# Optimization experiments

Hardware: AMD Instinct MI355X
Metric: run time of the kernel (lower is better)

The kernel has to match this reference:

```python
import jax, jax.numpy as jnp
import numpy as np

N_ENT, N_USR, N_ITEM, N_REL, N_CLS, N_FAC, D = 100000, 4096, 8192, 32, 3, 8, 128
N_EDGES, NNZ = 800000, 204800


def setup_inputs() -> dict:
    key = jax.random.key(0)
    ks = jax.random.split(key, 15)
    return {
        "entity_emb": jax.random.normal(ks[0], (N_ENT, D), jnp.float32),
        "item_emb": jax.random.normal(ks[1], (N_ITEM, D), jnp.float32),
        "user_emb": jax.random.normal(ks[2], (N_USR, D), jnp.float32),
        "latent_emb": jax.random.normal(ks[3], (N_FAC, D), jnp.float32),
        "relation_emb": jax.random.normal(ks[4], (N_REL, D), jnp.float32),
        "edge_index": jax.random.randint(ks[5], (2, N_EDGES), 0, N_ENT, jnp.int32),
        "edge_type": jax.random.randint(ks[6], (N_EDGES,), 0, N_REL, jnp.int32),
        "edge_imp": jax.random.uniform(ks[7], (N_EDGES,), jnp.float32),
        "inter_rows": jax.random.randint(ks[8], (NNZ,), 0, N_USR, jnp.int32),
        "inter_cols": jax.random.randint(ks[9], (NNZ,), 0, N_ENT, jnp.int32),
        "inter_vals": jax.random.uniform(ks[10], (NNZ,), jnp.float32),
        "disen_weight_att": jax.random.normal(ks[11], (N_FAC, N_REL), jnp.float32),
        "ent_rel_w": jax.random.normal(ks[12], (N_REL, D), jnp.float32),
        "usr_cls_w": jax.random.normal(ks[13], (N_CLS, D), jnp.float32),
        "inter_cls_mat": jax.random.normal(ks[14], (N_CLS, N_USR, N_ITEM), jnp.float32),
    }


def reference(entity_emb, item_emb, user_emb, latent_emb, relation_emb,
              edge_index, edge_type, edge_imp, inter_rows, inter_cols,
              inter_vals, disen_weight_att, ent_rel_w, usr_cls_w, inter_cls_mat):
    n_entities = entity_emb.shape[0]
    n_users = user_emb.shape[0]
    head, tail = edge_index[0], edge_index[1]

    # --- entity aggregation, e_mode='att_imp' ---
    # per-entity attention over relations: [n_ent, n_rel]
    ent_rel_att = jax.nn.softmax(entity_emb @ relation_emb.T, axis=1)
    mess_att = ent_rel_att[head, edge_type][:, None]              # [E,1]
    message_score = relation_emb[edge_type] * mess_att * edge_imp[:, None]  # [E,D]
    message = entity_emb[tail] * message_score                    # [E,D]
    entity_agg = jax.ops.segment_sum(message, head, num_segments=n_entities)

    # --- user aggregation, u_mode='inter_cls' ---
    # sparse interact_mat @ entity_emb via COO gather + segment_sum
    user_agg = jax.ops.segment_sum(entity_emb[inter_cols] * inter_vals[:, None],
                                   inter_rows, num_segments=n_users)
    user_cls_att = jax.nn.softmax(user_emb @ usr_cls_w.T, axis=1)  # [U,C]
    item_emb_2 = item_emb * relation_emb.sum(axis=0, keepdims=True)  # [I,D]
    # stack_c(inter_cls_mat[c] @ item_emb_2).transpose(0,1) -> [U,C,D]
    disen_weight = jnp.einsum('cui,id->ucd', inter_cls_mat, item_emb_2)
    user_agg = user_agg + (disen_weight * user_cls_att[:, :, None]).sum(axis=1)

    return entity_agg, user_agg
```

## Files before the change

kernel.cpp:

```cpp
#include <hip/hip_runtime.h>

#define N_ENT   100000
#define N_USR   4096
#define N_ITEM  8192
#define N_REL   32
#define N_CLS   3
#define DD      128
#define N_EDGES 800000
#define NNZ     204800

#define CAP_E   64
#define CAP_U   128

typedef __attribute__((ext_vector_type(8))) short short8;
typedef __attribute__((ext_vector_type(4))) float f32x4;

static __device__ __forceinline__ unsigned short f2bf(float x) {
    unsigned int u = __builtin_bit_cast(unsigned int, x);
    u = (u + 0x7fffu + ((u >> 16) & 1u)) >> 16;
    return (unsigned short)u;
}
static __device__ __forceinline__ float bflo(unsigned int v) {
    return __uint_as_float(v << 16);
}
static __device__ __forceinline__ float bfhi(unsigned int v) {
    return __uint_as_float(v & 0xffff0000u);
}

#define ZB  ((N_ENT + N_USR + 255) / 256)
#define EAB ((N_ENT + 255) / 256)

__global__ __launch_bounds__(256) void k_prep(const float* __restrict__ ent,
                                              const float* __restrict__ rel,
                                              float* __restrict__ att,
                                              unsigned short* __restrict__ entbf,
                                              unsigned short* __restrict__ relbf,
                                              int* __restrict__ cnt,
                                              const float* __restrict__ item,
                                              unsigned short* __restrict__ Bt,
                                              const float* __restrict__ usr,
                                              const float* __restrict__ w,
                                              float* __restrict__ uatt) {
    __shared__ float smem[N_REL * DD];
    int bx = blockIdx.x;

    if (bx < ZB) {
        int i = bx * 256 + threadIdx.x;
        if (i < N_ENT + N_USR) cnt[i] = 0;
        return;
    }
    bx -= ZB;

    if (bx < EAB) {
        for (int i = threadIdx.x; i < N_REL * DD; i += 256) smem[i] = rel[i];
        __syncthreads();
        if (bx == 0) {
            for (int i = threadIdx.x; i < N_REL * DD; i += 256)
                relbf[i] = f2bf(smem[i]);
        }
        int e = bx * 256 + threadIdx.x;
        if (e >= N_ENT) return;
        const float4* row = (const float4*)(ent + (size_t)e * DD);
        unsigned short* brow = entbf + (size_t)e * DD;
        float acc[N_REL];
#pragma unroll
        for (int r = 0; r < N_REL; ++r) acc[r] = 0.f;
        for (int dq = 0; dq < DD / 4; ++dq) {
            float4 v = row[dq];
            ushort4 bv;
            bv.x = f2bf(v.x); bv.y = f2bf(v.y); bv.z = f2bf(v.z); bv.w = f2bf(v.w);
            *(ushort4*)(brow + dq * 4) = bv;
#pragma unroll
            for (int r = 0; r < N_REL; ++r) {
                float4 ww = *(const float4*)&smem[r * DD + dq * 4];
                acc[r] += v.x * ww.x + v.y * ww.y + v.z * ww.z + v.w * ww.w;
            }
        }
        float m = acc[0];
#pragma unroll
        for (int r = 1; r < N_REL; ++r) m = fmaxf(m, acc[r]);
        float s = 0.f;
#pragma unroll
        for (int r = 0; r < N_REL; ++r) { acc[r] = __expf(acc[r] - m); s += acc[r]; }
        float inv = 1.f / s;
        float* o = att + (size_t)e * N_REL;
#pragma unroll
        for (int r = 0; r < N_REL; ++r) o[r] = acc[r] * inv;
        return;
    }
    bx -= EAB;

    if (bx < 1024) {
        float (*tile)[33] = (float(*)[33])smem;
        float* ssum = smem + 32 * 33;
        const int b2 = bx & 255, by = bx >> 8;
        const int tx = threadIdx.x & 31, ty = threadIdx.x >> 5;
        const int i0 = b2 * 32, d0 = by * 32;
        if (threadIdx.x < 32) {
            float s = 0.f;
            for (int r = 0; r < N_REL; ++r) s += rel[r * DD + d0 + threadIdx.x];
            ssum[threadIdx.x] = s;
        }
#pragma unroll
        for (int rr = 0; rr < 4; ++rr)
            tile[ty + 8 * rr][tx] = item[(size_t)(i0 + ty + 8 * rr) * DD + d0 + tx];
        __syncthreads();
#pragma unroll
        for (int rr = 0; rr < 4; ++rr) {
            int d = d0 + ty + 8 * rr;
            Bt[(size_t)d * N_ITEM + i0 + tx] = f2bf(tile[tx][ty + 8 * rr] * ssum[ty + 8 * rr]);
        }
        return;
    }
    bx -= 1024;

    {
        for (int i = threadIdx.x; i < N_CLS * DD; i += 256) smem[i] = w[i];
        __syncthreads();
        int u = bx * 256 + threadIdx.x;
        const float4* row = (const float4*)(usr + (size_t)u * DD);
        float acc[3] = {0.f, 0.f, 0.f};
        for (int dq = 0; dq < DD / 4; ++dq) {
            float4 v = row[dq];
#pragma unroll
            for (int c = 0; c < 3; ++c) {
                float4 ww = *(const float4*)&smem[c * DD + dq * 4];
                acc[c] += v.x * ww.x + v.y * ww.y + v.z * ww.z + v.w * ww.w;
            }
        }
        float m = fmaxf(acc[0], fmaxf(acc[1], acc[2]));
        float s = 0.f;
#pragma unroll
        for (int c = 0; c < 3; ++c) { acc[c] = __expf(acc[c] - m); s += acc[c]; }
        float inv = 1.f / s;
#pragma unroll
        for (int c = 0; c < 3; ++c) uatt[u * 3 + c] = acc[c] * inv;
    }
}

__global__ __launch_bounds__(256) void k_scatter2(const int* __restrict__ eidx,
                                                  const int* __restrict__ etyp,
                                                  const float* __restrict__ eimp,
                                                  const int* __restrict__ irow,
                                                  const int* __restrict__ icol,
                                                  const float* __restrict__ ival,
                                                  int* __restrict__ cnt,
                                                  int2* __restrict__ pack_e,
                                                  int2* __restrict__ pack_u) {
    int i = blockIdx.x * 256 + threadIdx.x;
    if (i < N_EDGES) {
        int h = eidx[i], tl = eidx[N_EDGES + i], r = etyp[i];
        int p = atomicAdd(&cnt[h], 1);
        if (p < CAP_E) {
            int2 pk;
            pk.x = tl | (r << 24);
            pk.y = __float_as_int(eimp[i]);
            pack_e[(size_t)h * CAP_E + p] = pk;
        }
    }
    if (i < NNZ) {
        int u = irow[i];
        int p = atomicAdd(&cnt[N_ENT + u], 1);
        if (p < CAP_U) {
            int2 pk;
            pk.x = icol[i];
            pk.y = __float_as_int(ival[i]);
            pack_u[(size_t)u * CAP_U + p] = pk;
        }
    }
}

__global__ __launch_bounds__(256) void k_edge_agg4(const unsigned short* __restrict__ entbf,
                                                   const unsigned short* __restrict__ relbf,
                                                   const float* __restrict__ att,
                                                   const int2* __restrict__ pack,
                                                   const int* __restrict__ cnt,
                                                   float* __restrict__ out) {
    const int lane = threadIdx.x & 63;
    const int wid = blockIdx.x * 4 + (threadIdx.x >> 6);
#pragma unroll 1
    for (int hh = 0; hh < 4; ++hh) {
        const int h = wid * 4 + hh;
        const int n = min(cnt[h], CAP_E);
        const float attv = att[(size_t)h * N_REL + (lane & 31)];
        const int2* seg = pack + (size_t)h * CAP_E;
        float ax = 0.f, ay = 0.f;
        for (int j = 0; j < n; j += 8) {
            int2 pk[8];
#pragma unroll
            for (int k = 0; k < 8; ++k) pk[k] = seg[min(j + k, n - 1)];
            unsigned int bv[8], rv[8];
            float sc[8];
#pragma unroll
            for (int k = 0; k < 8; ++k) {
                int r = ((unsigned)pk[k].x) >> 24;
                float s = __shfl(attv, r, 64) * __int_as_float(pk[k].y);
                sc[k] = (j + k < n) ? s : 0.f;
                bv[k] = ((const unsigned int*)(entbf + (size_t)(pk[k].x & 0xFFFFFF) * DD))[lane];
                rv[k] = ((const unsigned int*)(relbf + (size_t)r * DD))[lane];
            }
#pragma unroll
            for (int k = 0; k < 8; ++k) {
                ax = fmaf(bflo(rv[k]) * bflo(bv[k]), sc[k], ax);
                ay = fmaf(bfhi(rv[k]) * bfhi(bv[k]), sc[k], ay);
            }
        }
        float2 o; o.x = ax; o.y = ay;
        ((float2*)(out + (size_t)h * DD))[lane] = o;
    }
}

#define BM 64
#define BK 32
#define SPLITK 16
#define KCH (N_ITEM / SPLITK)
#define PLANE ((long long)N_USR * N_ITEM)

__global__ __launch_bounds__(256) void k_disen_gemm(const float* __restrict__ icm,
                                                    const unsigned short* __restrict__ Bt,
                                                    const float* __restrict__ uatt,
                                                    float* __restrict__ part) {
    __shared__ unsigned short sA[BM][40];
    __shared__ unsigned short sB[DD][40];

    const int t  = threadIdx.x;
    const int m0 = blockIdx.x * BM;
    const long long k0b = (long long)blockIdx.y * KCH;

    const int ua = t >> 3;
    const int qa = t & 7;
    const float a00 = uatt[(m0 + ua) * 3 + 0];
    const float a01 = uatt[(m0 + ua) * 3 + 1];
    const float a02 = uatt[(m0 + ua) * 3 + 2];
    const float a10 = uatt[(m0 + ua + 32) * 3 + 0];
    const float a11 = uatt[(m0 + ua + 32) * 3 + 1];
    const float a12 = uatt[(m0 + ua + 32) * 3 + 2];

    const int db = t >> 2;
    const int qb = t & 3;

    const int lane = t & 63;
    const int wv = t >> 6;
    const int wm = wv >> 1, wn = wv & 1;
    const int la = lane & 15, lb = lane >> 4;

    f32x4 acc[2][4];
#pragma unroll
    for (int mi = 0; mi < 2; ++mi)
#pragma unroll
        for (int ni = 0; ni < 4; ++ni) {
            f32x4 z = {0.f, 0.f, 0.f, 0.f};
            acc[mi][ni] = z;
        }

    float4 rA0[3], rA1[3];
    short8 rB0, rB1;
    {
        const long long base0 = (long long)(m0 + ua) * N_ITEM + k0b + qa * 4;
        rA0[0] = *(const float4*)(icm + base0);
        rA0[1] = *(const float4*)(icm + base0 + PLANE);
        rA0[2] = *(const float4*)(icm + base0 + 2 * PLANE);
        const long long base1 = base0 + 32ll * N_ITEM;
        rA1[0] = *(const float4*)(icm + base1);
        rA1[1] = *(const float4*)(icm + base1 + PLANE);
        rA1[2] = *(const float4*)(icm + base1 + 2 * PLANE);
        const unsigned short* g0 = Bt + (long long)db * N_ITEM + k0b + qb * 8;
        rB0 = *(const short8*)g0;
        rB1 = *(const short8*)(g0 + 64ll * N_ITEM);
    }

    for (int kk = 0; kk < KCH; kk += BK) {
        __syncthreads();
        {
            ushort4 p;
            p.x = f2bf(a00 * rA0[0].x + a01 * rA0[1].x + a02 * rA0[2].x);
            p.y = f2bf(a00 * rA0[0].y + a01 * rA0[1].y + a02 * rA0[2].y);
            p.z = f2bf(a00 * rA0[0].z + a01 * rA0[1].z + a02 * rA0[2].z);
            p.w = f2bf(a00 * rA0[0].w + a01 * rA0[1].w + a02 * rA0[2].w);
            *(ushort4*)(&sA[ua][0] + qa * 4) = p;
            p.x = f2bf(a10 * rA1[0].x + a11 * rA1[1].x + a12 * rA1[2].x);
            p.y = f2bf(a10 * rA1[0].y + a11 * rA1[1].y + a12 * rA1[2].y);
            p.z = f2bf(a10 * rA1[0].z + a11 * rA1[1].z + a12 * rA1[2].z);
            p.w = f2bf(a10 * rA1[0].w + a11 * rA1[1].w + a12 * rA1[2].w);
            *(ushort4*)(&sA[ua + 32][0] + qa * 4) = p;
            *(short8*)(&sB[db][0] + qb * 8) = rB0;
            *(short8*)(&sB[db + 64][0] + qb * 8) = rB1;
        }
        __syncthreads();

        if (kk + BK < KCH) {
            const long long k0 = k0b + kk + BK;
            const long long base0 = (long long)(m0 + ua) * N_ITEM + k0 + qa * 4;
            rA0[0] = *(const float4*)(icm + base0);
            rA0[1] = *(const float4*)(icm + base0 + PLANE);
            rA0[2] = *(const float4*)(icm + base0 + 2 * PLANE);
            const long long base1 = base0 + 32ll * N_ITEM;
            rA1[0] = *(const float4*)(icm + base1);
            rA1[1] = *(const float4*)(icm + base1 + PLANE);
            rA1[2] = *(const float4*)(icm + base1 + 2 * PLANE);
            const unsigned short* g0 = Bt + (long long)db * N_ITEM + k0 + qb * 8;
            rB0 = *(const short8*)g0;
            rB1 = *(const short8*)(g0 + 64ll * N_ITEM);
        }

        short8 af[2], bfr[4];
#pragma unroll
        for (int mi = 0; mi < 2; ++mi)
            af[mi] = *(const short8*)(&sA[wm * 32 + mi * 16 + la][0] + lb * 8);
#pragma unroll
        for (int ni = 0; ni < 4; ++ni)
            bfr[ni] = *(const short8*)(&sB[wn * 64 + ni * 16 + la][0] + lb * 8);
#pragma unroll
        for (int mi = 0; mi < 2; ++mi)
#pragma unroll
            for (int ni = 0; ni < 4; ++ni)
                acc[mi][ni] = __builtin_amdgcn_mfma_f32_16x16x32_bf16(
                    af[mi], bfr[ni], acc[mi][ni], 0, 0, 0);
    }

    float* pbase = part + (size_t)blockIdx.y * ((size_t)N_USR * DD);
#pragma unroll
    for (int mi = 0; mi < 2; ++mi)
#pragma unroll
        for (int ni = 0; ni < 4; ++ni)
#pragma unroll
            for (int r = 0; r < 4; ++r) {
                int row = m0 + wm * 32 + mi * 16 + lb * 4 + r;
                int col = wn * 64 + ni * 16 + la;
                pbase[(size_t)row * DD + col] = acc[mi][ni][r];
            }
}

__global__ __launch_bounds__(256) void k_user_final(const unsigned short* __restrict__ entbf,
                                                    const int2* __restrict__ pack,
                                                    const int* __restrict__ cnt,
                                                    const float* __restrict__ part,
                                                    float* __restrict__ uout) {
    const int lane = threadIdx.x & 63;
    const int u = blockIdx.x * 4 + (threadIdx.x >> 6);
    const int n = min(cnt[N_ENT + u], CAP_U);
    const int2* seg = pack + (size_t)u * CAP_U;
    float ax = 0.f, ay = 0.f;
    for (int j = 0; j < n; j += 8) {
        int2 pk[8];
#pragma unroll
        for (int k = 0; k < 8; ++k) pk[k] = seg[min(j + k, n - 1)];
        unsigned int bv[8];
        float sc[8];
#pragma unroll
        for (int k = 0; k < 8; ++k) {
            sc[k] = (j + k < n) ? __int_as_float(pk[k].y) : 0.f;
            bv[k] = ((const unsigned int*)(entbf + (size_t)pk[k].x * DD))[lane];
        }
#pragma unroll
        for (int k = 0; k < 8; ++k) {
            ax = fmaf(bflo(bv[k]), sc[k], ax);
            ay = fmaf(bfhi(bv[k]), sc[k], ay);
        }
    }
#pragma unroll
    for (int k = 0; k < SPLITK; ++k) {
        float2 p = ((const float2*)(part + (size_t)k * N_USR * DD + (size_t)u * DD))[lane];
        ax += p.x;
        ay += p.y;
    }
    float2 o; o.x = ax; o.y = ay;
    ((float2*)(uout + (size_t)u * DD))[lane] = o;
}

static constexpr size_t algn(size_t x) { return (x + 255) & ~(size_t)255; }

extern "C" void kernel_launch(void* const* d_in, const int* in_sizes, int n_in,
                              void* d_out, int out_size, void* d_ws, size_t ws_size,
                              hipStream_t stream) {
    const float* ent  = (const float*)d_in[0];
    const float* item = (const float*)d_in[1];
    const float* usr  = (const float*)d_in[2];
    const float* rel  = (const float*)d_in[4];
    const int*   eidx = (const int*)d_in[5];
    const int*   etyp = (const int*)d_in[6];
    const float* eimp = (const float*)d_in[7];
    const int*   irow = (const int*)d_in[8];
    const int*   icol = (const int*)d_in[9];
    const float* ival = (const float*)d_in[10];
    const float* uclw = (const float*)d_in[13];
    const float* icm  = (const float*)d_in[14];

    float* out_ent = (float*)d_out;
    float* out_usr = out_ent + (size_t)N_ENT * DD;

    char* w = (char*)d_ws;
    size_t o = 0;
    float* ws_att  = (float*)(w + o);  o = algn(o + (size_t)N_ENT * N_REL * 4);
    float* ws_uatt = (float*)(w + o);  o = algn(o + (size_t)N_USR * N_CLS * 4);
    unsigned short* ws_Bt    = (unsigned short*)(w + o); o = algn(o + (size_t)DD * N_ITEM * 2);
    unsigned short* ws_entbf = (unsigned short*)(w + o); o = algn(o + (size_t)N_ENT * DD * 2);
    unsigned short* ws_relbf = (unsigned short*)(w + o); o = algn(o + (size_t)N_REL * DD * 2);
    int*  ws_cnt   = (int*)(w + o);  o = algn(o + (size_t)(N_ENT + N_USR) * 4);
    int2* pack_e   = (int2*)(w + o); o = algn(o + (size_t)N_ENT * CAP_E * 8);
    int2* pack_u   = (int2*)(w + o); o = algn(o + (size_t)N_USR * CAP_U * 8);
    float* part    = (float*)(w + o); o = algn(o + (size_t)SPLITK * N_USR * DD * 4);

    (void)in_sizes; (void)n_in; (void)ws_size; (void)out_size;

    k_prep<<<ZB + EAB + 1024 + 16, 256, 0, stream>>>(ent, rel, ws_att, ws_entbf, ws_relbf,
                                                     ws_cnt, item, ws_Bt, usr, uclw, ws_uatt);
    k_scatter2<<<(N_EDGES + 255) / 256, 256, 0, stream>>>(eidx, etyp, eimp, irow, icol, ival,
                                                          ws_cnt, pack_e, pack_u);
    k_edge_agg4<<<N_ENT / 16, 256, 0, stream>>>(ws_entbf, ws_relbf, ws_att,
                                                pack_e, ws_cnt, out_ent);
    k_disen_gemm<<<dim3(N_USR / BM, SPLITK), 256, 0, stream>>>(icm, ws_Bt, ws_uatt, part);
    k_user_final<<<N_USR / 4, 256, 0, stream>>>(ws_entbf, pack_u, ws_cnt, part, out_usr);
}
```

Baseline: 323.8 us.

## Merge independent kernels into two heterogeneous launches to overlap GEMM and scatter

Combines the disentangle GEMM and the edge/interaction scatter into one launch, with blocks branching on block index, and likewise merges edge aggregation with the user final reduction. The aim is to remove launch gaps and tail underutilization by letting the compute-bound GEMM overlap with the atomic-heavy scatter, and the gather kernels overlap with each other. The cost is that every block reserves the GEMM shared memory and register budget, which can lower occupancy for the scatter blocks. The edge loop's unroll-1 pragma also becomes a full unroll.

```diff
diff --git a/kernel.cpp b/kernel.cpp
--- a/kernel.cpp
+++ b/kernel.cpp
@@ -138,159 +138,68 @@
     }
 }
 
-__global__ __launch_bounds__(256) void k_scatter2(const int* __restrict__ eidx,
-                                                  const int* __restrict__ etyp,
-                                                  const float* __restrict__ eimp,
-                                                  const int* __restrict__ irow,
-                                                  const int* __restrict__ icol,
-                                                  const float* __restrict__ ival,
-                                                  int* __restrict__ cnt,
-                                                  int2* __restrict__ pack_e,
-                                                  int2* __restrict__ pack_u) {
-    int i = blockIdx.x * 256 + threadIdx.x;
-    if (i < N_EDGES) {
-        int h = eidx[i], tl = eidx[N_EDGES + i], r = etyp[i];
-        int p = atomicAdd(&cnt[h], 1);
-        if (p < CAP_E) {
-            int2 pk;
-            pk.x = tl | (r << 24);
-            pk.y = __float_as_int(eimp[i]);
-            pack_e[(size_t)h * CAP_E + p] = pk;
-        }
-    }
-    if (i < NNZ) {
-        int u = irow[i];
-        int p = atomicAdd(&cnt[N_ENT + u], 1);
-        if (p < CAP_U) {
-            int2 pk;
-            pk.x = icol[i];
-            pk.y = __float_as_int(ival[i]);
-            pack_u[(size_t)u * CAP_U + p] = pk;
-        }
-    }
-}
-
-__global__ __launch_bounds__(256) void k_edge_agg4(const unsigned short* __restrict__ entbf,
-                                                   const unsigned short* __restrict__ relbf,
-                                                   const float* __restrict__ att,
-                                                   const int2* __restrict__ pack,
-                                                   const int* __restrict__ cnt,
-                                                   float* __restrict__ out) {
-    const int lane = threadIdx.x & 63;
-    const int wid = blockIdx.x * 4 + (threadIdx.x >> 6);
-#pragma unroll 1
-    for (int hh = 0; hh < 4; ++hh) {
-        const int h = wid * 4 + hh;
-        const int n = min(cnt[h], CAP_E);
-        const float attv = att[(size_t)h * N_REL + (lane & 31)];
-        const int2* seg = pack + (size_t)h * CAP_E;
-        float ax = 0.f, ay = 0.f;
-        for (int j = 0; j < n; j += 8) {
-            int2 pk[8];
-#pragma unroll
-            for (int k = 0; k < 8; ++k) pk[k] = seg[min(j + k, n - 1)];
-            unsigned int bv[8], rv[8];
-            float sc[8];
-#pragma unroll
-            for (int k = 0; k < 8; ++k) {
-                int r = ((unsigned)pk[k].x) >> 24;
-                float s = __shfl(attv, r, 64) * __int_as_float(pk[k].y);
-                sc[k] = (j + k < n) ? s : 0.f;
-                bv[k] = ((const unsigned int*)(entbf + (size_t)(pk[k].x & 0xFFFFFF) * DD))[lane];
-                rv[k] = ((const unsigned int*)(relbf + (size_t)r * DD))[lane];
-            }
-#pragma unroll
-            for (int k = 0; k < 8; ++k) {
-                ax = fmaf(bflo(rv[k]) * bflo(bv[k]), sc[k], ax);
-                ay = fmaf(bfhi(rv[k]) * bfhi(bv[k]), sc[k], ay);
-            }
-        }
-        float2 o; o.x = ax; o.y = ay;
-        ((float2*)(out + (size_t)h * DD))[lane] = o;
-    }
-}
-
 #define BM 64
 #define BK 32
 #define SPLITK 16
 #define KCH (N_ITEM / SPLITK)
 #define PLANE ((long long)N_USR * N_ITEM)
-
-__global__ __launch_bounds__(256) void k_disen_gemm(const float* __restrict__ icm,
-                                                    const unsigned short* __restrict__ Bt,
-                                                    const float* __restrict__ uatt,
-                                                    float* __restrict__ part) {
-    __shared__ unsigned short sA[BM][40];
-    __shared__ unsigned short sB[DD][40];
-
-    const int t  = threadIdx.x;
-    const int m0 = blockIdx.x * BM;
-    const long long k0b = (long long)blockIdx.y * KCH;
-
-    const int ua = t >> 3;
-    const int qa = t & 7;
-    const float a00 = uatt[(m0 + ua) * 3 + 0];
-    const float a01 = uatt[(m0 + ua) * 3 + 1];
-    const float a02 = uatt[(m0 + ua) * 3 + 2];
-    const float a10 = uatt[(m0 + ua + 32) * 3 + 0];
-    const float a11 = uatt[(m0 + ua + 32) * 3 + 1];
-    const float a12 = uatt[(m0 + ua + 32) * 3 + 2];
-
-    const int db = t >> 2;
-    const int qb = t & 3;
-
-    const int lane = t & 63;
-    const int wv = t >> 6;
-    const int wm = wv >> 1, wn = wv & 1;
-    const int la = lane & 15, lb = lane >> 4;
-
-    f32x4 acc[2][4];
-#pragma unroll
-    for (int mi = 0; mi < 2; ++mi)
-#pragma unroll
-        for (int ni = 0; ni < 4; ++ni) {
-            f32x4 z = {0.f, 0.f, 0.f, 0.f};
-            acc[mi][ni] = z;
-        }
-
-    float4 rA0[3], rA1[3];
-    short8 rB0, rB1;
-    {
-        const long long base0 = (long long)(m0 + ua) * N_ITEM + k0b + qa * 4;
-        rA0[0] = *(const float4*)(icm + base0);
-        rA0[1] = *(const float4*)(icm + base0 + PLANE);
-        rA0[2] = *(const float4*)(icm + base0 + 2 * PLANE);
-        const long long base1 = base0 + 32ll * N_ITEM;
-        rA1[0] = *(const float4*)(icm + base1);
-        rA1[1] = *(const float4*)(icm + base1 + PLANE);
-        rA1[2] = *(const float4*)(icm + base1 + 2 * PLANE);
-        const unsigned short* g0 = Bt + (long long)db * N_ITEM + k0b + qb * 8;
-        rB0 = *(const short8*)g0;
-        rB1 = *(const short8*)(g0 + 64ll * N_ITEM);
-    }
-
-    for (int kk = 0; kk < KCH; kk += BK) {
-        __syncthreads();
+#define GEMM_BLOCKS ((N_USR / BM) * SPLITK)
+#define SCAT_BLOCKS ((N_EDGES + 255) / 256)
+
+__global__ __launch_bounds__(256) void k_node2(const float* __restrict__ icm,
+                                               const unsigned short* __restrict__ Bt,
+                                               const float* __restrict__ uatt,
+                                               float* __restrict__ part,
+                                               const int* __restrict__ eidx,
+                                               const int* __restrict__ etyp,
+                                               const float* __restrict__ eimp,
+                                               const int* __restrict__ irow,
+                                               const int* __restrict__ icol,
+                                               const float* __restrict__ ival,
+                                               int* __restrict__ cnt,
+                                               int2* __restrict__ pack_e,
+                                               int2* __restrict__ pack_u) {
+    __shared__ unsigned short smem[BM * 40 + DD * 40];
+
+    if (blockIdx.x < GEMM_BLOCKS) {
+        unsigned short (*sA)[40] = (unsigned short(*)[40])smem;
+        unsigned short (*sB)[40] = (unsigned short(*)[40])(smem + BM * 40);
+
+        const int t  = threadIdx.x;
+        const int m0 = (blockIdx.x & 63) * BM;
+        const int ky = blockIdx.x >> 6;
+        const long long k0b = (long long)ky * KCH;
+
+        const int ua = t >> 3;
+        const int qa = t & 7;
+        const float a00 = uatt[(m0 + ua) * 3 + 0];
+        const float a01 = uatt[(m0 + ua) * 3 + 1];
+        const float a02 = uatt[(m0 + ua) * 3 + 2];
+        const float a10 = uatt[(m0 + ua + 32) * 3 + 0];
+        const float a11 = uatt[(m0 + ua + 32) * 3 + 1];
+        const float a12 = uatt[(m0 + ua + 32) * 3 + 2];
+
+        const int db = t >> 2;
+        const int qb = t & 3;
+
+        const int lane = t & 63;
+        const int wv = t >> 6;
+        const int wm = wv >> 1, wn = wv & 1;
+        const int la = lane & 15, lb = lane >> 4;
+
+        f32x4 acc[2][4];
+#pragma unroll
+        for (int mi = 0; mi < 2; ++mi)
+#pragma unroll
+            for (int ni = 0; ni < 4; ++ni) {
+                f32x4 z = {0.f, 0.f, 0.f, 0.f};
+                acc[mi][ni] = z;
+            }
+
+        float4 rA0[3], rA1[3];
+        short8 rB0, rB1;
         {
-            ushort4 p;
-            p.x = f2bf(a00 * rA0[0].x + a01 * rA0[1].x + a02 * rA0[2].x);
-            p.y = f2bf(a00 * rA0[0].y + a01 * rA0[1].y + a02 * rA0[2].y);
-            p.z = f2bf(a00 * rA0[0].z + a01 * rA0[1].z + a02 * rA0[2].z);
-            p.w = f2bf(a00 * rA0[0].w + a01 * rA0[1].w + a02 * rA0[2].w);
-            *(ushort4*)(&sA[ua][0] + qa * 4) = p;
-            p.x = f2bf(a10 * rA1[0].x + a11 * rA1[1].x + a12 * rA1[2].x);
-            p.y = f2bf(a10 * rA1[0].y + a11 * rA1[1].y + a12 * rA1[2].y);
-            p.z = f2bf(a10 * rA1[0].z + a11 * rA1[1].z + a12 * rA1[2].z);
-            p.w = f2bf(a10 * rA1[0].w + a11 * rA1[1].w + a12 * rA1[2].w);
-            *(ushort4*)(&sA[ua + 32][0] + qa * 4) = p;
-            *(short8*)(&sB[db][0] + qb * 8) = rB0;
-            *(short8*)(&sB[db + 64][0] + qb * 8) = rB1;
-        }
-        __syncthreads();
-
-        if (kk + BK < KCH) {
-            const long long k0 = k0b + kk + BK;
-            const long long base0 = (long long)(m0 + ua) * N_ITEM + k0 + qa * 4;
+            const long long base0 = (long long)(m0 + ua) * N_ITEM + k0b + qa * 4;
             rA0[0] = *(const float4*)(icm + base0);
             rA0[1] = *(const float4*)(icm + base0 + PLANE);
             rA0[2] = *(const float4*)(icm + base0 + 2 * PLANE);
@@ -298,74 +207,173 @@
             rA1[0] = *(const float4*)(icm + base1);
             rA1[1] = *(const float4*)(icm + base1 + PLANE);
             rA1[2] = *(const float4*)(icm + base1 + 2 * PLANE);
-            const unsigned short* g0 = Bt + (long long)db * N_ITEM + k0 + qb * 8;
+            const unsigned short* g0 = Bt + (long long)db * N_ITEM + k0b + qb * 8;
             rB0 = *(const short8*)g0;
             rB1 = *(const short8*)(g0 + 64ll * N_ITEM);
         }
 
-        short8 af[2], bfr[4];
+        for (int kk = 0; kk < KCH; kk += BK) {
+            __syncthreads();
+            {
+                ushort4 p;
+                p.x = f2bf(a00 * rA0[0].x + a01 * rA0[1].x + a02 * rA0[2].x);
+                p.y = f2bf(a00 * rA0[0].y + a01 * rA0[1].y + a02 * rA0[2].y);
+                p.z = f2bf(a00 * rA0[0].z + a01 * rA0[1].z + a02 * rA0[2].z);
+                p.w = f2bf(a00 * rA0[0].w + a01 * rA0[1].w + a02 * rA0[2].w);
+                *(ushort4*)(&sA[ua][0] + qa * 4) = p;
+                p.x = f2bf(a10 * rA1[0].x + a11 * rA1[1].x + a12 * rA1[2].x);
+                p.y = f2bf(a10 * rA1[0].y + a11 * rA1[1].y + a12 * rA1[2].y);
+                p.z = f2bf(a10 * rA1[0].z + a11 * rA1[1].z + a12 * rA1[2].z);
+                p.w = f2bf(a10 * rA1[0].w + a11 * rA1[1].w + a12 * rA1[2].w);
+                *(ushort4*)(&sA[ua + 32][0] + qa * 4) = p;
+                *(short8*)(&sB[db][0] + qb * 8) = rB0;
+                *(short8*)(&sB[db + 64][0] + qb * 8) = rB1;
+            }
+            __syncthreads();
+
+            if (kk + BK < KCH) {
+                const long long k0 = k0b + kk + BK;
+                const long long base0 = (long long)(m0 + ua) * N_ITEM + k0 + qa * 4;
+                rA0[0] = *(const float4*)(icm + base0);
+                rA0[1] = *(const float4*)(icm + base0 + PLANE);
+                rA0[2] = *(const float4*)(icm + base0 + 2 * PLANE);
+                const long long base1 = base0 + 32ll * N_ITEM;
+                rA1[0] = *(const float4*)(icm + base1);
+                rA1[1] = *(const float4*)(icm + base1 + PLANE);
+                rA1[2] = *(const float4*)(icm + base1 + 2 * PLANE);
+                const unsigned short* g0 = Bt + (long long)db * N_ITEM + k0 + qb * 8;
+                rB0 = *(const short8*)g0;
+                rB1 = *(const short8*)(g0 + 64ll * N_ITEM);
+            }
+
+            short8 af[2], bfr[4];
+#pragma unroll
+            for (int mi = 0; mi < 2; ++mi)
+                af[mi] = *(const short8*)(&sA[wm * 32 + mi * 16 + la][0] + lb * 8);
+#pragma unroll
+            for (int ni = 0; ni < 4; ++ni)
+                bfr[ni] = *(const short8*)(&sB[wn * 64 + ni * 16 + la][0] + lb * 8);
+#pragma unroll
+            for (int mi = 0; mi < 2; ++mi)
+#pragma unroll
+                for (int ni = 0; ni < 4; ++ni)
+                    acc[mi][ni] = __builtin_amdgcn_mfma_f32_16x16x32_bf16(
+                        af[mi], bfr[ni], acc[mi][ni], 0, 0, 0);
+        }
+
+        float* pbase = part + (size_t)ky * ((size_t)N_USR * DD);
 #pragma unroll
         for (int mi = 0; mi < 2; ++mi)
-            af[mi] = *(const short8*)(&sA[wm * 32 + mi * 16 + la][0] + lb * 8);
-#pragma unroll
-        for (int ni = 0; ni < 4; ++ni)
-            bfr[ni] = *(const short8*)(&sB[wn * 64 + ni * 16 + la][0] + lb * 8);
-#pragma unroll
-        for (int mi = 0; mi < 2; ++mi)
 #pragma unroll
             for (int ni = 0; ni < 4; ++ni)
-                acc[mi][ni] = __builtin_amdgcn_mfma_f32_16x16x32_bf16(
-                    af[mi], bfr[ni], acc[mi][ni], 0, 0, 0);
-    }
-
-    float* pbase = part + (size_t)blockIdx.y * ((size_t)N_USR * DD);
-#pragma unroll
-    for (int mi = 0; mi < 2; ++mi)
-#pragma unroll
-        for (int ni = 0; ni < 4; ++ni)
-#pragma unroll
-            for (int r = 0; r < 4; ++r) {
-                int row = m0 + wm * 32 + mi * 16 + lb * 4 + r;
-                int col = wn * 64 + ni * 16 + la;
-                pbase[(size_t)row * DD + col] = acc[mi][ni][r];
-            }
-}
-
-__global__ __launch_bounds__(256) void k_user_final(const unsigned short* __restrict__ entbf,
-                                                    const int2* __restrict__ pack,
-                                                    const int* __restrict__ cnt,
-                                                    const float* __restrict__ part,
-                                                    float* __restrict__ uout) {
+#pragma unroll
+                for (int r = 0; r < 4; ++r) {
+                    int row = m0 + wm * 32 + mi * 16 + lb * 4 + r;
+                    int col = wn * 64 + ni * 16 + la;
+                    pbase[(size_t)row * DD + col] = acc[mi][ni][r];
+                }
+    } else {
+        int i = (blockIdx.x - GEMM_BLOCKS) * 256 + threadIdx.x;
+        if (i < N_EDGES) {
+            int h = eidx[i], tl = eidx[N_EDGES + i], r = etyp[i];
+            int p = atomicAdd(&cnt[h], 1);
+            if (p < CAP_E) {
+                int2 pk;
+                pk.x = tl | (r << 24);
+                pk.y = __float_as_int(eimp[i]);
+                pack_e[(size_t)h * CAP_E + p] = pk;
+            }
+        }
+        if (i < NNZ) {
+            int u = irow[i];
+            int p = atomicAdd(&cnt[N_ENT + u], 1);
+            if (p < CAP_U) {
+                int2 pk;
+                pk.x = icol[i];
+                pk.y = __float_as_int(ival[i]);
+                pack_u[(size_t)u * CAP_U + p] = pk;
+            }
+        }
+    }
+}
+
+#define EDGE_BLOCKS (N_ENT / 16)
+#define USER_BLOCKS (N_USR / 4)
+
+__global__ __launch_bounds__(256) void k_node3(const unsigned short* __restrict__ entbf,
+                                               const unsigned short* __restrict__ relbf,
+                                               const float* __restrict__ att,
+                                               const int2* __restrict__ pack_e,
+                                               const int2* __restrict__ pack_u,
+                                               const int* __restrict__ cnt,
+                                               const float* __restrict__ part,
+                                               float* __restrict__ out_ent,
+                                               float* __restrict__ out_usr) {
     const int lane = threadIdx.x & 63;
-    const int u = blockIdx.x * 4 + (threadIdx.x >> 6);
-    const int n = min(cnt[N_ENT + u], CAP_U);
-    const int2* seg = pack + (size_t)u * CAP_U;
-    float ax = 0.f, ay = 0.f;
-    for (int j = 0; j < n; j += 8) {
-        int2 pk[8];
-#pragma unroll
-        for (int k = 0; k < 8; ++k) pk[k] = seg[min(j + k, n - 1)];
-        unsigned int bv[8];
-        float sc[8];
-#pragma unroll
-        for (int k = 0; k < 8; ++k) {
-            sc[k] = (j + k < n) ? __int_as_float(pk[k].y) : 0.f;
-            bv[k] = ((const unsigned int*)(entbf + (size_t)pk[k].x * DD))[lane];
-        }
-#pragma unroll
-        for (int k = 0; k < 8; ++k) {
-            ax = fmaf(bflo(bv[k]), sc[k], ax);
-            ay = fmaf(bfhi(bv[k]), sc[k], ay);
-        }
-    }
-#pragma unroll
-    for (int k = 0; k < SPLITK; ++k) {
-        float2 p = ((const float2*)(part + (size_t)k * N_USR * DD + (size_t)u * DD))[lane];
-        ax += p.x;
-        ay += p.y;
-    }
-    float2 o; o.x = ax; o.y = ay;
-    ((float2*)(uout + (size_t)u * DD))[lane] = o;
+
+    if (blockIdx.x < EDGE_BLOCKS) {
+        const int wid = blockIdx.x * 4 + (threadIdx.x >> 6);
+#pragma unroll
+        for (int hh = 0; hh < 4; ++hh) {
+            const int h = wid * 4 + hh;
+            const int n = min(cnt[h], CAP_E);
+            const float attv = att[(size_t)h * N_REL + (lane & 31)];
+            const int2* seg = pack_e + (size_t)h * CAP_E;
+            float ax = 0.f, ay = 0.f;
+            for (int j = 0; j < n; j += 8) {
+                int2 pk[8];
+#pragma unroll
+                for (int k = 0; k < 8; ++k) pk[k] = seg[min(j + k, n - 1)];
+                unsigned int bv[8], rv[8];
+                float sc[8];
+#pragma unroll
+                for (int k = 0; k < 8; ++k) {
+                    int r = ((unsigned)pk[k].x) >> 24;
+                    float s = __shfl(attv, r, 64) * __int_as_float(pk[k].y);
+                    sc[k] = (j + k < n) ? s : 0.f;
+                    bv[k] = ((const unsigned int*)(entbf + (size_t)(pk[k].x & 0xFFFFFF) * DD))[lane];
+                    rv[k] = ((const unsigned int*)(relbf + (size_t)r * DD))[lane];
+                }
+#pragma unroll
+                for (int k = 0; k < 8; ++k) {
+                    ax = fmaf(bflo(rv[k]) * bflo(bv[k]), sc[k], ax);
+                    ay = fmaf(bfhi(rv[k]) * bfhi(bv[k]), sc[k], ay);
+                }
+            }
+            float2 o; o.x = ax; o.y = ay;
+            ((float2*)(out_ent + (size_t)h * DD))[lane] = o;
+        }
+    } else {
+        const int u = (blockIdx.x - EDGE_BLOCKS) * 4 + (threadIdx.x >> 6);
+        const int n = min(cnt[N_ENT + u], CAP_U);
+        const int2* seg = pack_u + (size_t)u * CAP_U;
+        float ax = 0.f, ay = 0.f;
+        for (int j = 0; j < n; j += 8) {
+            int2 pk[8];
+#pragma unroll
+            for (int k = 0; k < 8; ++k) pk[k] = seg[min(j + k, n - 1)];
+            unsigned int bv[8];
+            float sc[8];
+#pragma unroll
+            for (int k = 0; k < 8; ++k) {
+                sc[k] = (j + k < n) ? __int_as_float(pk[k].y) : 0.f;
+                bv[k] = ((const unsigned int*)(entbf + (size_t)pk[k].x * DD))[lane];
+            }
+#pragma unroll
+            for (int k = 0; k < 8; ++k) {
+                ax = fmaf(bflo(bv[k]), sc[k], ax);
+                ay = fmaf(bfhi(bv[k]), sc[k], ay);
+            }
+        }
+#pragma unroll
+        for (int k = 0; k < SPLITK; ++k) {
+            float2 p = ((const float2*)(part + (size_t)k * N_USR * DD + (size_t)u * DD))[lane];
+            ax += p.x;
+            ay += p.y;
+        }
+        float2 o; o.x = ax; o.y = ay;
+        ((float2*)(out_usr + (size_t)u * DD))[lane] = o;
+    }
 }
 
 static constexpr size_t algn(size_t x) { return (x + 255) & ~(size_t)255; }
@@ -405,10 +413,10 @@
 
     k_prep<<<ZB + EAB + 1024 + 16, 256, 0, stream>>>(ent, rel, ws_att, ws_entbf, ws_relbf,
                                                      ws_cnt, item, ws_Bt, usr, uclw, ws_uatt);
-    k_scatter2<<<(N_EDGES + 255) / 256, 256, 0, stream>>>(eidx, etyp, eimp, irow, icol, ival,
-                                                          ws_cnt, pack_e, pack_u);
-    k_edge_agg4<<<N_ENT / 16, 256, 0, stream>>>(ws_entbf, ws_relbf, ws_att,
-                                                pack_e, ws_cnt, out_ent);
-    k_disen_gemm<<<dim3(N_USR / BM, SPLITK), 256, 0, stream>>>(icm, ws_Bt, ws_uatt, part);
-    k_user_final<<<N_USR / 4, 256, 0, stream>>>(ws_entbf, pack_u, ws_cnt, part, out_usr);
-}
+    k_node2<<<GEMM_BLOCKS + SCAT_BLOCKS, 256, 0, stream>>>(icm, ws_Bt, ws_uatt, part,
+                                                           eidx, etyp, eimp, irow, icol, ival,
+                                                           ws_cnt, pack_e, pack_u);
+    k_node3<<<EDGE_BLOCKS + USER_BLOCKS, 256, 0, stream>>>(ws_entbf, ws_relbf, ws_att,
+                                                           pack_e, pack_u, ws_cnt, part,
+                                                           out_ent, out_usr);
+}
```

Result: faster. 313.8 us (-3.1%).
